# Kernel optimization log

Measured on AMD Instinct MI355X. Metric: run time of the kernel, lower is better.

The kernel has to match this reference:

```python
import jax, jax.numpy as jnp
import numpy as np

N_AGENTS = 8
N_ACTIONS = 16
SAMPLE = 16
STATE_DIM = 256
EMBED = 256
IN_DIM = N_AGENTS * N_ACTIONS + STATE_DIM  # 384


def setup_inputs() -> dict:
    key = jax.random.key(0)
    ks = jax.random.split(key, 12)
    bs, t = 32, 32
    s = 0.05
    return {
        "states": jax.random.normal(ks[0], (bs, t, STATE_DIM), jnp.float32),
        "agent_qs": jax.random.normal(ks[1], (bs, t, N_AGENTS, N_ACTIONS), jnp.float32),
        "W1": jax.random.normal(ks[2], (IN_DIM, EMBED), jnp.float32) * s,
        "b1": jnp.zeros((EMBED,), jnp.float32),
        "W2": jax.random.normal(ks[3], (EMBED, EMBED), jnp.float32) * s,
        "b2": jnp.zeros((EMBED,), jnp.float32),
        "W3": jax.random.normal(ks[4], (EMBED, 1), jnp.float32) * s,
        "b3": jnp.zeros((1,), jnp.float32),
        "Vw1": jax.random.normal(ks[5], (STATE_DIM, EMBED), jnp.float32) * s,
        "Vb1": jnp.zeros((EMBED,), jnp.float32),
        "Vw2": jax.random.normal(ks[6], (EMBED, 1), jnp.float32) * s,
        "Vb2": jnp.zeros((1,), jnp.float32),
    }


def reference(states, agent_qs, W1, b1, W2, b2, W3, b3, Vw1, Vb1, Vw2, Vb2):
    bs, t = states.shape[0], states.shape[1]
    B = bs * t
    A, NA, S, sd = N_AGENTS, N_ACTIONS, SAMPLE, STATE_DIM
    st = states.reshape(B, sd)
    qs = agent_qs.reshape(B, A, NA)

    # --- sample grand coalitions (random permutation per (B,S) row) ---
    perm_key = jax.random.key(42)
    u = jax.random.uniform(perm_key, (B, S, A))
    pos = jnp.argsort(u, axis=-1)          # grand_coalitions_pos: agent i -> position pos[i]
    inv = jnp.argsort(pos, axis=-1)        # grand_coalitions: position j -> agent inv[j]

    indiv = jax.nn.one_hot(pos, A, dtype=st.dtype)                         # (B,S,A,A)
    subcoal = (jnp.arange(A)[None, None, None, :] <= pos[..., None]).astype(st.dtype)
    no_i = subcoal - indiv                                                 # coalition members excl. self

    # reorder agent qs along position dim: reordered[b,s,j,:] = qs[b, inv[b,s,j], :]
    reordered = jnp.take_along_axis(
        jnp.broadcast_to(qs[:, None], (B, S, A, NA)), inv[..., None], axis=2)

    # (B,S,A,A,NA): detach contribution of other coalition members
    coal = (jax.lax.stop_gradient(reordered[:, :, None] * no_i[..., None])
            + reordered[:, :, None] * indiv[..., None])

    x = coal.reshape(B * S * A, A * NA)
    stx = jnp.broadcast_to(st[:, None, None], (B, S, A, sd)).reshape(B * S * A, sd)
    inp = jnp.concatenate([stx, x], axis=1)

    h = jax.nn.relu(inp @ W1 + b1)
    h = jax.nn.relu(h @ W2 + b2)
    advs = h @ W3 + b3
    v = jax.nn.relu(stx @ Vw1 + Vb1) @ Vw2 + Vb2

    marginal = (advs + v).reshape(B, S, A)
    shapley = marginal.mean(axis=1)        # mean over samples
    return shapley.reshape(bs, t, A)
```

## Files before the change

### kernel.cpp

```cpp
#include <hip/hip_runtime.h>


#define A_N   8
#define NA_N  16
#define S_N   16
#define SD    256
#define EMB   256
#define B_TOT 1024

typedef __bf16 bf16x8 __attribute__((ext_vector_type(8)));
typedef float  f32x4  __attribute__((ext_vector_type(4)));

__device__ __forceinline__ f32x4 splat4(float v) {
  f32x4 x; x[0] = v; x[1] = v; x[2] = v; x[3] = v; return x;
}
__device__ __forceinline__ bf16x8 zero8() {
  bf16x8 z;
#pragma unroll
  for (int j = 0; j < 8; ++j) z[j] = (__bf16)0.0f;
  return z;
}

__device__ __forceinline__ float jax_uniform(unsigned idx) {
  const unsigned ks0 = 0u, ks1 = 42u, ks2 = 0x1BD11BDAu ^ 42u;
  unsigned x0 = 0u + ks0;
  unsigned x1 = idx + ks1;
#define TF_RND(r) { x0 += x1; x1 = (x1 << (r)) | (x1 >> (32 - (r))); x1 ^= x0; }
  TF_RND(13) TF_RND(15) TF_RND(26) TF_RND(6)  x0 += ks1; x1 += ks2 + 1u;
  TF_RND(17) TF_RND(29) TF_RND(16) TF_RND(24) x0 += ks2; x1 += ks0 + 2u;
  TF_RND(13) TF_RND(15) TF_RND(26) TF_RND(6)  x0 += ks0; x1 += ks1 + 3u;
  TF_RND(17) TF_RND(29) TF_RND(16) TF_RND(24) x0 += ks1; x1 += ks2 + 4u;
  TF_RND(13) TF_RND(15) TF_RND(26) TF_RND(6)  x0 += ks2; x1 += ks0 + 5u;
#undef TF_RND
  const unsigned bits = x0 ^ x1;
  return __uint_as_float((bits >> 9) | 0x3F800000u) - 1.0f;
}

__global__ __launch_bounds__(256) void prep_pack_kernel(
    const float* __restrict__ states, const float* __restrict__ W1,
    const float* __restrict__ b1, const float* __restrict__ W2,
    const float* __restrict__ Vw1, const float* __restrict__ Vb1,
    const float* __restrict__ Vw2, float* __restrict__ sW,
    float* __restrict__ vpart, __bf16* __restrict__ W1b_bf,
    __bf16* __restrict__ W2_bf) {
  const int n = threadIdx.x;

  if (blockIdx.x < 48) {
    const int ts = blockIdx.x * 256 + n;
    if (ts < 4096) {
      const int t = ts >> 10, rem = ts & 1023, u = rem >> 6, L = rem & 63;
      const int q = L >> 4, l15 = L & 15;
#pragma unroll
      for (int j = 0; j < 8; ++j) {
        const int k = t * 32 + q * 8 + j, nn = u * 16 + l15;
        W1b_bf[ts * 8 + j] = (__bf16)W1[(SD + k) * EMB + nn];
      }
    } else {
      const int ts2 = ts - 4096;
      const int t = ts2 >> 10, rem = ts2 & 1023, u = rem >> 6, L = rem & 63;
      const int q = L >> 4, l15 = L & 15;
#pragma unroll
      for (int j = 0; j < 8; ++j) {
        const int k = t * 32 + q * 8 + j, nn = u * 16 + l15;
        W2_bf[ts2 * 8 + j] = (__bf16)W2[k * EMB + nn];
      }
    }
    return;
  }

  __shared__ float vred[4][64];
  const int blk = blockIdx.x - 48;
  const int mi = blk >> 2;
  const int ni = blk & 3;
  const int w = n >> 6, L = n & 63, q = L >> 4, l15 = L & 15;

  f32x4 acc[4][2];
#pragma unroll
  for (int ui = 0; ui < 2; ++ui) {
    const int col = (ni * 8 + w * 2 + ui) * 16 + l15;
    const float bias = (col < EMB) ? b1[col] : Vb1[col - EMB];
#pragma unroll
    for (int mt = 0; mt < 4; ++mt) acc[mt][ui] = splat4(bias);
  }

#pragma unroll 2
  for (int t = 0; t < 8; ++t) {
    bf16x8 bfr[2];
#pragma unroll
    for (int ui = 0; ui < 2; ++ui) {
      const int nn = (ni * 8 + w * 2 + ui) * 16 + l15;
#pragma unroll
      for (int j = 0; j < 8; ++j) {
        const int k = t * 32 + q * 8 + j;
        const float v = (nn < EMB) ? W1[k * EMB + nn]
                                   : Vw1[k * EMB + (nn - EMB)];
        bfr[ui][j] = (__bf16)v;
      }
    }
#pragma unroll
    for (int mt = 0; mt < 4; ++mt) {
      const float* srow =
          &states[(mi * 64 + mt * 16 + l15) * SD + t * 32 + q * 8];
      bf16x8 af;
#pragma unroll
      for (int j = 0; j < 8; ++j) af[j] = (__bf16)srow[j];
#pragma unroll
      for (int ui = 0; ui < 2; ++ui)
        acc[mt][ui] = __builtin_amdgcn_mfma_f32_16x16x32_bf16(
            af, bfr[ui], acc[mt][ui], 0, 0, 0);
    }
  }

  if (ni < 2) {
#pragma unroll
    for (int ui = 0; ui < 2; ++ui) {
      const int col = (ni * 8 + w * 2 + ui) * 16 + l15;
#pragma unroll
      for (int mt = 0; mt < 4; ++mt)
#pragma unroll
        for (int r = 0; r < 4; ++r)
          sW[(mi * 64 + mt * 16 + q * 4 + r) * EMB + col] = acc[mt][ui][r];
    }
  } else {
#pragma unroll
    for (int mt = 0; mt < 4; ++mt) {
#pragma unroll
      for (int r = 0; r < 4; ++r) {
        float p = 0.f;
#pragma unroll
        for (int ui = 0; ui < 2; ++ui) {
          const int colV = (ni * 8 + w * 2 + ui) * 16 + l15 - EMB;
          p = fmaf(fmaxf(acc[mt][ui][r], 0.f), Vw2[colV], p);
        }
#pragma unroll
        for (int off = 1; off < 16; off <<= 1) p += __shfl_xor(p, off);
        if (l15 == 0) vred[w][mt * 16 + q * 4 + r] = p;
      }
    }
    __syncthreads();
    if (n < 64)
      vpart[(ni - 2) * B_TOT + mi * 64 + n] =
          vred[0][n] + vred[1][n] + vred[2][n] + vred[3][n];
  }
}

__global__ __launch_bounds__(256, 4) void main_kernel(
    const float* __restrict__ agent_qs, const float* __restrict__ b2g,
    const float* __restrict__ W3, const float* __restrict__ b3,
    const float* __restrict__ Vb2, const float* __restrict__ sW,
    const float* __restrict__ vpart, const __bf16* __restrict__ W1b_bf,
    const __bf16* __restrict__ W2_bf, float* __restrict__ out) {
  __shared__ bf16x8 h1_l[32 * 64];
  __shared__ __attribute__((aligned(16))) __bf16 qs_bf[A_N * NA_N];
  __shared__ float u_l[128];
  __shared__ int   inv_l[128];
  __shared__ int   pos_l[128];
  __shared__ float adv_part[4][128];

  const int b = blockIdx.x;
  const int n = threadIdx.x;
  const int w = n >> 6, L = n & 63, q = L >> 4, l15 = L & 15;

  if (n < 128) {
    qs_bf[n] = (__bf16)agent_qs[b * 128 + n];
    u_l[n] = jax_uniform((unsigned)(b * 128 + n));
  }
  float sWv[4], b2v[4], w3v[4];
#pragma unroll
  for (int j = 0; j < 4; ++j) {
    const int c = (w * 4 + j) * 16 + l15;
    sWv[j] = sW[b * EMB + c];
    b2v[j] = b2g[c];
    w3v[j] = W3[c];
  }
  __syncthreads();

  if (n < 128) {
    const int s = n >> 3, a = n & 7;
    const float u = u_l[n];
    int r = 0;
#pragma unroll
    for (int a2 = 0; a2 < A_N; ++a2) {
      const float u2 = u_l[s * 8 + a2];
      r += (u2 < u || (u2 == u && a2 < a)) ? 1 : 0;
    }
    inv_l[n] = r;
    pos_l[s * 8 + r] = a;
  }
  __syncthreads();

  const int i_pref  = l15 & 7;
  const int sl_half = l15 >> 3;
  const int jq      = q >> 1;
  const int na0     = (q & 1) * 8;

  for (int p = 0; p < 2; ++p) {
#pragma unroll 1
    for (int nh = 0; nh < 2; ++nh) {
      f32x4 acc[4][2];
#pragma unroll
      for (int i = 0; i < 2; ++i) {
#pragma unroll
        for (int mt = 0; mt < 4; ++mt) acc[mt][i] = splat4(sWv[nh * 2 + i]);
      }
#pragma unroll 2
      for (int t = 0; t < 4; ++t) {
        const int jcoal = t * 2 + jq;
        const bool on = (jcoal <= i_pref);
        bf16x8 bfr[2];
#pragma unroll
        for (int i = 0; i < 2; ++i)
          bfr[i] = *(const bf16x8*)
              &W1b_bf[((t * 16 + w * 4 + nh * 2 + i) * 64 + L) * 8];
#pragma unroll
        for (int mt = 0; mt < 4; ++mt) {
          const int ag = inv_l[(p * 8 + mt * 2 + sl_half) * 8 + jcoal];
          const bf16x8 qv = *(const bf16x8*)&qs_bf[ag * NA_N + na0];
          const bf16x8 af = on ? qv : zero8();
#pragma unroll
          for (int i = 0; i < 2; ++i)
            acc[mt][i] = __builtin_amdgcn_mfma_f32_16x16x32_bf16(
                af, bfr[i], acc[mt][i], 0, 0, 0);
        }
      }
      __bf16* h1e = (__bf16*)h1_l;
#pragma unroll
      for (int i = 0; i < 2; ++i) {
        const int c = (w * 4 + nh * 2 + i) * 16 + l15;
        const int t2 = c >> 5, q2 = (c >> 3) & 3, j2 = l15 & 7;
#pragma unroll
        for (int mt = 0; mt < 4; ++mt) {
#pragma unroll
          for (int r = 0; r < 4; ++r) {
            const float v = fmaxf(acc[mt][i][r], 0.f);
            h1e[(((t2 * 4 + mt) * 64) + q2 * 16 + q * 4 + r) * 8 + j2] =
                (__bf16)v;
          }
        }
      }
    }
    __syncthreads();

    float psum[4][4];
#pragma unroll
    for (int mt = 0; mt < 4; ++mt)
#pragma unroll
      for (int r = 0; r < 4; ++r) psum[mt][r] = 0.f;

#pragma unroll 1
    for (int nh = 0; nh < 2; ++nh) {
      f32x4 acc[4][2];
#pragma unroll
      for (int i = 0; i < 2; ++i) {
#pragma unroll
        for (int mt = 0; mt < 4; ++mt) acc[mt][i] = splat4(b2v[nh * 2 + i]);
      }
#pragma unroll 2
      for (int t = 0; t < 8; ++t) {
        bf16x8 bfr[2];
#pragma unroll
        for (int i = 0; i < 2; ++i)
          bfr[i] = *(const bf16x8*)
              &W2_bf[((t * 16 + w * 4 + nh * 2 + i) * 64 + L) * 8];
#pragma unroll
        for (int mt = 0; mt < 4; ++mt) {
          const bf16x8 af = h1_l[(t * 4 + mt) * 64 + L];
#pragma unroll
          for (int i = 0; i < 2; ++i)
            acc[mt][i] = __builtin_amdgcn_mfma_f32_16x16x32_bf16(
                af, bfr[i], acc[mt][i], 0, 0, 0);
        }
      }
#pragma unroll
      for (int i = 0; i < 2; ++i) {
#pragma unroll
        for (int mt = 0; mt < 4; ++mt)
#pragma unroll
          for (int r = 0; r < 4; ++r)
            psum[mt][r] = fmaf(fmaxf(acc[mt][i][r], 0.f), w3v[nh * 2 + i],
                               psum[mt][r]);
      }
    }

#pragma unroll
    for (int mt = 0; mt < 4; ++mt) {
#pragma unroll
      for (int r = 0; r < 4; ++r) {
        float sum = psum[mt][r];
#pragma unroll
        for (int off = 1; off < 16; off <<= 1) sum += __shfl_xor(sum, off);
        if (l15 == 0) adv_part[w][p * 64 + mt * 16 + q * 4 + r] = sum;
      }
    }
    __syncthreads();
  }

  if (n < A_N) {
    float sh = 0.f;
#pragma unroll
    for (int s = 0; s < S_N; ++s) {
      const int idx = (s >> 3) * 64 + (s & 7) * 8 + pos_l[s * 8 + n];
      sh += adv_part[0][idx] + adv_part[1][idx] +
            adv_part[2][idx] + adv_part[3][idx];
    }
    out[b * A_N + n] = sh * (1.f / 16.f) + b3[0] + Vb2[0] +
                       vpart[b] + vpart[B_TOT + b];
  }
}

extern "C" void kernel_launch(void* const* d_in, const int* in_sizes, int n_in,
                              void* d_out, int out_size, void* d_ws,
                              size_t ws_size, hipStream_t stream) {
  const float* states   = (const float*)d_in[0];
  const float* agent_qs = (const float*)d_in[1];
  const float* W1       = (const float*)d_in[2];
  const float* b1       = (const float*)d_in[3];
  const float* W2       = (const float*)d_in[4];
  const float* b2       = (const float*)d_in[5];
  const float* W3       = (const float*)d_in[6];
  const float* b3       = (const float*)d_in[7];
  const float* Vw1      = (const float*)d_in[8];
  const float* Vb1      = (const float*)d_in[9];
  const float* Vw2      = (const float*)d_in[10];
  const float* Vb2      = (const float*)d_in[11];
  float* out = (float*)d_out;

  char* ws = (char*)d_ws;
  float*  sW     = (float*)(ws);
  float*  vpart  = (float*)(ws + 1048576);
  __bf16* W1b_bf = (__bf16*)(ws + 1057792);
  __bf16* W2_bf  = (__bf16*)(ws + 1123328);

  prep_pack_kernel<<<112, 256, 0, stream>>>(states, W1, b1, W2, Vw1, Vb1,
                                            Vw2, sW, vpart, W1b_bf, W2_bf);
  main_kernel<<<B_TOT, 256, 0, stream>>>(agent_qs, b2, W3, b3, Vb2, sW,
                                         vpart, W1b_bf, W2_bf, out);
}
```

Baseline: 123.9 us.

## Use 512-thread blocks so each wave owns two column tiles across all samples

The main kernel now runs 8 waves per block instead of 4. Each wave covers two 16-column output tiles for all 128 rows at once, replacing the earlier two-pass loop over row halves. The h1 shared buffer doubles to hold every row, and the advantage partials go to 8 per-wave slots. This removes one barrier round and reuses each weight fragment over 8 row tiles instead of 4. The costs are more shared memory and more registers per wave, which may cut occupancy.

```diff
diff --git a/kernel.cpp b/kernel.cpp
--- a/kernel.cpp
+++ b/kernel.cpp
@@ -144,18 +144,18 @@
   }
 }
 
-__global__ __launch_bounds__(256, 4) void main_kernel(
+__global__ __launch_bounds__(512, 4) void main_kernel(
     const float* __restrict__ agent_qs, const float* __restrict__ b2g,
     const float* __restrict__ W3, const float* __restrict__ b3,
     const float* __restrict__ Vb2, const float* __restrict__ sW,
     const float* __restrict__ vpart, const __bf16* __restrict__ W1b_bf,
     const __bf16* __restrict__ W2_bf, float* __restrict__ out) {
-  __shared__ bf16x8 h1_l[32 * 64];
+  __shared__ bf16x8 h1_l[64 * 64];
   __shared__ __attribute__((aligned(16))) __bf16 qs_bf[A_N * NA_N];
   __shared__ float u_l[128];
   __shared__ int   inv_l[128];
   __shared__ int   pos_l[128];
-  __shared__ float adv_part[4][128];
+  __shared__ float adv_part[8][128];
 
   const int b = blockIdx.x;
   const int n = threadIdx.x;
@@ -165,13 +165,13 @@
     qs_bf[n] = (__bf16)agent_qs[b * 128 + n];
     u_l[n] = jax_uniform((unsigned)(b * 128 + n));
   }
-  float sWv[4], b2v[4], w3v[4];
-#pragma unroll
-  for (int j = 0; j < 4; ++j) {
-    const int c = (w * 4 + j) * 16 + l15;
-    sWv[j] = sW[b * EMB + c];
-    b2v[j] = b2g[c];
-    w3v[j] = W3[c];
+  float sWv[2], b2v[2], w3v[2];
+#pragma unroll
+  for (int i = 0; i < 2; ++i) {
+    const int c = (w * 2 + i) * 16 + l15;
+    sWv[i] = sW[b * EMB + c];
+    b2v[i] = b2g[c];
+    w3v[i] = W3[c];
   }
   __syncthreads();
 
@@ -194,114 +194,90 @@
   const int jq      = q >> 1;
   const int na0     = (q & 1) * 8;
 
-  for (int p = 0; p < 2; ++p) {
 #pragma unroll 1
-    for (int nh = 0; nh < 2; ++nh) {
-      f32x4 acc[4][2];
-#pragma unroll
-      for (int i = 0; i < 2; ++i) {
-#pragma unroll
-        for (int mt = 0; mt < 4; ++mt) acc[mt][i] = splat4(sWv[nh * 2 + i]);
-      }
+  for (int i = 0; i < 2; ++i) {
+    const int u = w * 2 + i;
+    f32x4 acc[8];
+#pragma unroll
+    for (int mt = 0; mt < 8; ++mt) acc[mt] = splat4(sWv[i]);
 #pragma unroll 2
-      for (int t = 0; t < 4; ++t) {
-        const int jcoal = t * 2 + jq;
-        const bool on = (jcoal <= i_pref);
-        bf16x8 bfr[2];
-#pragma unroll
-        for (int i = 0; i < 2; ++i)
-          bfr[i] = *(const bf16x8*)
-              &W1b_bf[((t * 16 + w * 4 + nh * 2 + i) * 64 + L) * 8];
-#pragma unroll
-        for (int mt = 0; mt < 4; ++mt) {
-          const int ag = inv_l[(p * 8 + mt * 2 + sl_half) * 8 + jcoal];
-          const bf16x8 qv = *(const bf16x8*)&qs_bf[ag * NA_N + na0];
-          const bf16x8 af = on ? qv : zero8();
-#pragma unroll
-          for (int i = 0; i < 2; ++i)
-            acc[mt][i] = __builtin_amdgcn_mfma_f32_16x16x32_bf16(
-                af, bfr[i], acc[mt][i], 0, 0, 0);
-        }
-      }
-      __bf16* h1e = (__bf16*)h1_l;
-#pragma unroll
-      for (int i = 0; i < 2; ++i) {
-        const int c = (w * 4 + nh * 2 + i) * 16 + l15;
-        const int t2 = c >> 5, q2 = (c >> 3) & 3, j2 = l15 & 7;
-#pragma unroll
-        for (int mt = 0; mt < 4; ++mt) {
-#pragma unroll
-          for (int r = 0; r < 4; ++r) {
-            const float v = fmaxf(acc[mt][i][r], 0.f);
-            h1e[(((t2 * 4 + mt) * 64) + q2 * 16 + q * 4 + r) * 8 + j2] =
-                (__bf16)v;
-          }
-        }
-      }
-    }
-    __syncthreads();
-
-    float psum[4][4];
-#pragma unroll
-    for (int mt = 0; mt < 4; ++mt)
-#pragma unroll
-      for (int r = 0; r < 4; ++r) psum[mt][r] = 0.f;
+    for (int t = 0; t < 4; ++t) {
+      const int jcoal = t * 2 + jq;
+      const bool on = (jcoal <= i_pref);
+      const bf16x8 bfr = *(const bf16x8*)&W1b_bf[((t * 16 + u) * 64 + L) * 8];
+#pragma unroll
+      for (int mt = 0; mt < 8; ++mt) {
+        const int ag = inv_l[(mt * 2 + sl_half) * 8 + jcoal];
+        const bf16x8 qv = *(const bf16x8*)&qs_bf[ag * NA_N + na0];
+        const bf16x8 af = on ? qv : zero8();
+        acc[mt] = __builtin_amdgcn_mfma_f32_16x16x32_bf16(af, bfr, acc[mt],
+                                                          0, 0, 0);
+      }
+    }
+    __bf16* h1e = (__bf16*)h1_l;
+    const int c = u * 16 + l15;
+    const int t2 = c >> 5, q2 = (c >> 3) & 3, j2 = l15 & 7;
+#pragma unroll
+    for (int mt = 0; mt < 8; ++mt) {
+#pragma unroll
+      for (int r = 0; r < 4; ++r) {
+        const float v = fmaxf(acc[mt][r], 0.f);
+        h1e[(((t2 * 8 + mt) * 64) + q2 * 16 + q * 4 + r) * 8 + j2] = (__bf16)v;
+      }
+    }
+  }
+  __syncthreads();
+
+  float psum[8][4];
+#pragma unroll
+  for (int mt = 0; mt < 8; ++mt)
+#pragma unroll
+    for (int r = 0; r < 4; ++r) psum[mt][r] = 0.f;
 
 #pragma unroll 1
-    for (int nh = 0; nh < 2; ++nh) {
-      f32x4 acc[4][2];
-#pragma unroll
-      for (int i = 0; i < 2; ++i) {
-#pragma unroll
-        for (int mt = 0; mt < 4; ++mt) acc[mt][i] = splat4(b2v[nh * 2 + i]);
-      }
+  for (int i = 0; i < 2; ++i) {
+    const int u = w * 2 + i;
+    f32x4 acc[8];
+#pragma unroll
+    for (int mt = 0; mt < 8; ++mt) acc[mt] = splat4(b2v[i]);
 #pragma unroll 2
-      for (int t = 0; t < 8; ++t) {
-        bf16x8 bfr[2];
-#pragma unroll
-        for (int i = 0; i < 2; ++i)
-          bfr[i] = *(const bf16x8*)
-              &W2_bf[((t * 16 + w * 4 + nh * 2 + i) * 64 + L) * 8];
-#pragma unroll
-        for (int mt = 0; mt < 4; ++mt) {
-          const bf16x8 af = h1_l[(t * 4 + mt) * 64 + L];
-#pragma unroll
-          for (int i = 0; i < 2; ++i)
-            acc[mt][i] = __builtin_amdgcn_mfma_f32_16x16x32_bf16(
-                af, bfr[i], acc[mt][i], 0, 0, 0);
-        }
-      }
-#pragma unroll
-      for (int i = 0; i < 2; ++i) {
-#pragma unroll
-        for (int mt = 0; mt < 4; ++mt)
-#pragma unroll
-          for (int r = 0; r < 4; ++r)
-            psum[mt][r] = fmaf(fmaxf(acc[mt][i][r], 0.f), w3v[nh * 2 + i],
-                               psum[mt][r]);
-      }
-    }
-
-#pragma unroll
-    for (int mt = 0; mt < 4; ++mt) {
-#pragma unroll
-      for (int r = 0; r < 4; ++r) {
-        float sum = psum[mt][r];
-#pragma unroll
-        for (int off = 1; off < 16; off <<= 1) sum += __shfl_xor(sum, off);
-        if (l15 == 0) adv_part[w][p * 64 + mt * 16 + q * 4 + r] = sum;
-      }
-    }
-    __syncthreads();
-  }
+    for (int t = 0; t < 8; ++t) {
+      const bf16x8 bfr = *(const bf16x8*)&W2_bf[((t * 16 + u) * 64 + L) * 8];
+#pragma unroll
+      for (int mt = 0; mt < 8; ++mt) {
+        const bf16x8 af = h1_l[(t * 8 + mt) * 64 + L];
+        acc[mt] = __builtin_amdgcn_mfma_f32_16x16x32_bf16(af, bfr, acc[mt],
+                                                          0, 0, 0);
+      }
+    }
+#pragma unroll
+    for (int mt = 0; mt < 8; ++mt)
+#pragma unroll
+      for (int r = 0; r < 4; ++r)
+        psum[mt][r] = fmaf(fmaxf(acc[mt][r], 0.f), w3v[i], psum[mt][r]);
+  }
+
+#pragma unroll
+  for (int mt = 0; mt < 8; ++mt) {
+#pragma unroll
+    for (int r = 0; r < 4; ++r) {
+      float sum = psum[mt][r];
+#pragma unroll
+      for (int off = 1; off < 16; off <<= 1) sum += __shfl_xor(sum, off);
+      if (l15 == 0) adv_part[w][mt * 16 + q * 4 + r] = sum;
+    }
+  }
+  __syncthreads();
 
   if (n < A_N) {
     float sh = 0.f;
 #pragma unroll
     for (int s = 0; s < S_N; ++s) {
-      const int idx = (s >> 3) * 64 + (s & 7) * 8 + pos_l[s * 8 + n];
-      sh += adv_part[0][idx] + adv_part[1][idx] +
-            adv_part[2][idx] + adv_part[3][idx];
+      const int idx = s * 8 + pos_l[s * 8 + n];
+      float v = 0.f;
+#pragma unroll
+      for (int ww = 0; ww < 8; ++ww) v += adv_part[ww][idx];
+      sh += v;
     }
     out[b * A_N + n] = sh * (1.f / 16.f) + b3[0] + Vb2[0] +
                        vpart[b] + vpart[B_TOT + b];
@@ -333,6 +309,6 @@
 
   prep_pack_kernel<<<112, 256, 0, stream>>>(states, W1, b1, W2, Vw1, Vb1,
                                             Vw2, sW, vpart, W1b_bf, W2_bf);
-  main_kernel<<<B_TOT, 256, 0, stream>>>(agent_qs, b2, W3, b3, Vb2, sW,
+  main_kernel<<<B_TOT, 512, 0, stream>>>(agent_qs, b2, W3, b3, Vb2, sW,
                                          vpart, W1b_bf, W2_bf, out);
 }
```

Result: slower. 147.2 us (+18.8%).
